# Performance work log

Hardware: AMD Instinct MI355X
Metric: run time of the kernel (lower is better)

The kernel has to match this reference:

```python
import jax, jax.numpy as jnp
import numpy as np

BN_EPS = 1e-5

def _bn(x, g, b, m, v):
    # eval-mode BatchNorm1d over channel dim of [B, C, N]
    scale = g / jnp.sqrt(v + BN_EPS)
    return (x - m[:, None]) * scale[:, None] + b[:, None]

def _conv1(W, x, b=None):
    # 1x1 Conv1d == channel matmul: W [O, C], x [B, C, N] -> [B, O, N]
    y = jnp.einsum('oc,bcn->bon', W, x)
    if b is not None:
        y = y + b[:, None]
    return y

def _sa_layer(x, wqk, wv, bv, wt, bt, g, b, m, v):
    # offset self-attention; q_conv and k_conv share weights
    xk = _conv1(wqk, x)                          # [B, D, N]
    xq = jnp.swapaxes(xk, 1, 2)                  # [B, N, D]
    xv = _conv1(wv, x, bv)                       # [B, D, N]
    energy = jnp.einsum('bnd,bdm->bnm', xq, xk)  # [B, N, N]
    attn = jax.nn.softmax(energy, axis=-1)
    attn = attn / (1e-9 + attn.sum(axis=1, keepdims=True))  # L1 renorm over dim=1
    x_r = jnp.einsum('bdn,bnm->bdm', xv, attn)   # [B, D, N]
    x_r = jax.nn.relu(_bn(_conv1(wt, x - x_r, bt), g, b, m, v))
    return x + x_r

def setup_inputs() -> dict:
    key = jax.random.key(0)
    ks = iter(jax.random.split(key, 64))
    B, Cin, N = 16, 3, 2048
    D, F, H1, OUT = 128, 1024, 512, 50
    def rn(shape, s=0.05):
        return jax.random.normal(next(ks), shape, dtype=jnp.float32) * s
    def var(shape):
        return jax.random.uniform(next(ks), shape, dtype=jnp.float32) * 0.5 + 0.5
    inp = {
        'x': jax.random.normal(next(ks), (B, Cin, N), dtype=jnp.float32),
        'w1': rn((D, Cin)), 'w2': rn((D, D)),
        'bn1_g': jnp.ones((D,)), 'bn1_b': jnp.zeros((D,)), 'bn1_m': rn((D,)), 'bn1_v': var((D,)),
        'bn2_g': jnp.ones((D,)), 'bn2_b': jnp.zeros((D,)), 'bn2_m': rn((D,)), 'bn2_v': var((D,)),
        'sa_wqk': rn((4, D, D)), 'sa_wv': rn((4, D, D)), 'sa_bv': rn((4, D)),
        'sa_wt': rn((4, D, D)), 'sa_bt': rn((4, D)),
        'sa_g': jnp.ones((4, D)), 'sa_b': jnp.zeros((4, D)), 'sa_m': rn((4, D)), 'sa_v': var((4, D)),
        'wf': rn((F, 4 * D)),
        'bnf_g': jnp.ones((F,)), 'bnf_b': jnp.zeros((F,)), 'bnf_m': rn((F,)), 'bnf_v': var((F,)),
        'ws1': rn((H1, 3 * F)), 'bs1': rn((H1,)),
        'bns1_g': jnp.ones((H1,)), 'bns1_b': jnp.zeros((H1,)), 'bns1_m': rn((H1,)), 'bns1_v': var((H1,)),
        'ws2': rn((OUT, H1)), 'bs2': rn((OUT,)),
        'bns2_g': jnp.ones((OUT,)), 'bns2_b': jnp.zeros((OUT,)), 'bns2_m': rn((OUT,)), 'bns2_v': var((OUT,)),
    }
    return inp

def reference(x, w1, w2, bn1_g, bn1_b, bn1_m, bn1_v, bn2_g, bn2_b, bn2_m, bn2_v,
              sa_wqk, sa_wv, sa_bv, sa_wt, sa_bt, sa_g, sa_b, sa_m, sa_v,
              wf, bnf_g, bnf_b, bnf_m, bnf_v,
              ws1, bs1, bns1_g, bns1_b, bns1_m, bns1_v,
              ws2, bs2, bns2_g, bns2_b, bns2_m, bns2_v):
    B, _, N = x.shape
    h = jax.nn.relu(_bn(_conv1(w1, x), bn1_g, bn1_b, bn1_m, bn1_v))
    h = jax.nn.relu(_bn(_conv1(w2, h), bn2_g, bn2_b, bn2_m, bn2_v))
    feats = []
    for i in range(4):
        h = _sa_layer(h, sa_wqk[i], sa_wv[i], sa_bv[i], sa_wt[i], sa_bt[i],
                      sa_g[i], sa_b[i], sa_m[i], sa_v[i])
        feats.append(h)
    cat = jnp.concatenate(feats, axis=1)                 # [B, 512, N]
    fused = _bn(_conv1(wf, cat), bnf_g, bnf_b, bnf_m, bnf_v)
    fused = jnp.where(fused >= 0, fused, 0.2 * fused)    # LeakyReLU(0.2)
    x_max = fused.max(axis=2)                            # [B, 1024]
    x_avg = fused.mean(axis=2)                           # [B, 1024]
    gmax = jnp.broadcast_to(x_max[:, :, None], (B, x_max.shape[1], N))
    gavg = jnp.broadcast_to(x_avg[:, :, None], (B, x_avg.shape[1], N))
    h = jnp.concatenate([fused, gmax, gavg], axis=1)     # [B, 3072, N]
    h = jax.nn.relu(_bn(_conv1(ws1, h, bs1), bns1_g, bns1_b, bns1_m, bns1_v))
    # dropout is identity in eval mode
    h = jax.nn.relu(_bn(_conv1(ws2, h, bs2), bns2_g, bns2_b, bns2_m, bns2_v))
    return h  # [B, out_channel, N]
```

## Files before the change

### kernel.cpp

```cpp
#include <hip/hip_runtime.h>
#include <cstdint>
#include <cstddef>

#define B_   16
#define N_   2048
#define D_   128
#define F_   1024
#define H1_  512
#define OUT_ 50

static constexpr float BN_EPS = 1e-5f;

typedef __attribute__((ext_vector_type(8))) short short8;
typedef __attribute__((ext_vector_type(4))) float f32x4;

__device__ inline unsigned short f2bf(float f) {
  union { float f; unsigned u; } v; v.f = f;
  unsigned r = v.u + 0x7fff + ((v.u >> 16) & 1);
  return (unsigned short)(r >> 16);
}
__device__ inline float bf2f(unsigned short h) {
  union { unsigned u; float f; } v; v.u = ((unsigned)h) << 16; return v.f;
}

__device__ inline void dma16(const unsigned short* g, unsigned short* l) {
  __builtin_amdgcn_global_load_lds(
      (const __attribute__((address_space(1))) unsigned int*)g,
      (__attribute__((address_space(3))) unsigned int*)l, 16, 0, 0);
}

__global__ void foldw_k(const float* __restrict__ W, int ldW,
                        const float* __restrict__ bias,
                        const float* __restrict__ g, const float* __restrict__ bb,
                        const float* __restrict__ m, const float* __restrict__ v,
                        unsigned short* __restrict__ Wb, float* __restrict__ biasF,
                        int O, int Opad, int K) {
  long i = (long)blockIdx.x * 256 + threadIdx.x;
  if (i >= (long)Opad * K) return;
  int o = (int)(i / K), k = (int)(i % K);
  float sc = 1.f, sh = 0.f;
  if (o < O && g) { sc = g[o] * rsqrtf(v[o] + BN_EPS); sh = bb[o] - m[o] * sc; }
  float w = (o < O) ? W[(long)o * ldW + k] * sc : 0.f;
  Wb[i] = f2bf(w);
  if (k == 0 && biasF) {
    float bf = 0.f;
    if (o < O) bf = (bias ? bias[o] : 0.f) * sc + sh;
    biasF[o] = bf;
  }
}

__global__ void conv1_k(const float* __restrict__ x, const float* __restrict__ w1,
                        const float* __restrict__ g, const float* __restrict__ bb,
                        const float* __restrict__ m, const float* __restrict__ v,
                        unsigned short* __restrict__ h0b) {
  int o = threadIdx.x, n = blockIdx.x, b = blockIdx.y;
  const float* xb = x + (long)b * 3 * N_;
  float val = w1[o * 3 + 0] * xb[n] + w1[o * 3 + 1] * xb[N_ + n] + w1[o * 3 + 2] * xb[2 * N_ + n];
  float sc = g[o] * rsqrtf(v[o] + BN_EPS);
  val = val * sc + (bb[o] - m[o] * sc);
  h0b[((long)b * N_ + n) * D_ + o] = f2bf(fmaxf(val, 0.f));
}

template <int TM>
__global__ __launch_bounds__(256, 4)
void gemm_tok(const unsigned short* __restrict__ Wb, int ldW,
              const unsigned short* __restrict__ A, long sA, int ldA,
              const float* __restrict__ biasF,
              const float* __restrict__ perBO, int ldPBO,
              const unsigned short* __restrict__ resH, long sRes, int ldRes,
              unsigned short* __restrict__ outH, long sOutH, int ldOutH,
              float* __restrict__ pmax, float* __restrict__ psum,
              int K, int act, int flags) {
  constexpr int MT = TM / 32;
  __shared__ unsigned short lAB[TM * 64 + 128 * 64];
  __shared__ float lpm[4][64], lps[4][64];
  unsigned short* lA = lAB;
  unsigned short* lB = lAB + TM * 64;
  unsigned short* lS = lAB;
  int tid = threadIdx.x;
  int n0 = blockIdx.x * TM, o0 = blockIdx.y * 128, b = blockIdx.z;
  int wave = tid >> 6, lane = tid & 63;
  int wr = wave >> 1, wc = wave & 1;
  int quad = lane >> 4, l15 = lane & 15;
  int rowL = lane >> 3;
  int kseg = (lane & 7) ^ rowL;
  const unsigned short* Ab = A + (long)b * sA + (long)n0 * ldA;
  const unsigned short* Wp = Wb + (long)o0 * ldW;

  f32x4 acc[MT][4];
  #pragma unroll
  for (int i = 0; i < MT; ++i)
    #pragma unroll
    for (int j = 0; j < 4; ++j) acc[i][j] = (f32x4){0.f, 0.f, 0.f, 0.f};

  for (int kc = 0; kc < K; kc += 64) {
    #pragma unroll
    for (int t = 0; t < 4; ++t) {
      int chunk = t * 4 + wave;
      dma16(Wp + (long)(chunk * 8 + rowL) * ldW + kc + kseg * 8, &lB[chunk * 512]);
      if (chunk < TM / 8)
        dma16(Ab + (long)(chunk * 8 + rowL) * ldA + kc + kseg * 8, &lA[chunk * 512]);
    }
    __syncthreads();
    #pragma unroll
    for (int kk = 0; kk < 2; ++kk) {
      short8 af[MT], bf[4];
      #pragma unroll
      for (int mt = 0; mt < MT; ++mt) {
        int r = wr * (TM / 2) + mt * 16 + l15;
        af[mt] = *(const short8*)&lA[r * 64 + (((kk * 4 + quad) ^ (l15 & 7)) * 8)];
      }
      #pragma unroll
      for (int ot = 0; ot < 4; ++ot) {
        int r = wc * 64 + ot * 16 + l15;
        bf[ot] = *(const short8*)&lB[r * 64 + (((kk * 4 + quad) ^ (l15 & 7)) * 8)];
      }
      #pragma unroll
      for (int mt = 0; mt < MT; ++mt)
        #pragma unroll
        for (int ot = 0; ot < 4; ++ot)
          acc[mt][ot] = __builtin_amdgcn_mfma_f32_16x16x32_bf16(bf[ot], af[mt], acc[mt][ot], 0, 0, 0);
    }
    __syncthreads();
  }

  bool doPool = (flags & 32) != 0;
  #pragma unroll
  for (int ot = 0; ot < 4; ++ot) {
    int obL = wc * 64 + ot * 16 + quad * 4;
    int ob = o0 + obL;
    float bi[4] = {0.f, 0.f, 0.f, 0.f};
    if (biasF) { float4 t = *(const float4*)&biasF[ob]; bi[0] = t.x; bi[1] = t.y; bi[2] = t.z; bi[3] = t.w; }
    if (perBO) {
      float4 t = *(const float4*)&perBO[(long)b * ldPBO + ob];
      bi[0] += t.x; bi[1] += t.y; bi[2] += t.z; bi[3] += t.w;
    }
    float pm4[4], ps4[4];
    #pragma unroll
    for (int r = 0; r < 4; ++r) { pm4[r] = -1e30f; ps4[r] = 0.f; }
    int g = obL >> 3, go = obL & 7;
    #pragma unroll
    for (int mt = 0; mt < MT; ++mt) {
      int nL = wr * (TM / 2) + mt * 16 + l15;
      float vals[4];
      #pragma unroll
      for (int r = 0; r < 4; ++r) {
        float val = acc[mt][ot][r] + bi[r];
        if (act == 1)      val = fmaxf(val, 0.f);
        else if (act == 2) val = (val >= 0.f) ? val : 0.2f * val;
        vals[r] = val;
      }
      if (flags & 16) {
        uint2 rv = *(const uint2*)&resH[(long)b * sRes + (long)(n0 + nL) * ldRes + ob];
        unsigned short rr[4];
        *(uint2*)rr = rv;
        #pragma unroll
        for (int r = 0; r < 4; ++r) vals[r] += bf2f(rr[r]);
      }
      unsigned short t4[4];
      #pragma unroll
      for (int r = 0; r < 4; ++r) {
        t4[r] = f2bf(vals[r]);
        if (doPool) { pm4[r] = fmaxf(pm4[r], vals[r]); ps4[r] += vals[r]; }
      }
      int gp = (g & 8) | ((g ^ (nL & 7)) & 7);
      *(uint2*)&lS[nL * 128 + gp * 8 + go] = *(uint2*)&t4[0];
    }
    if (doPool) {
      #pragma unroll
      for (int r = 0; r < 4; ++r) {
        float m = pm4[r], s = ps4[r];
        m = fmaxf(m, __shfl_xor(m, 1)); s += __shfl_xor(s, 1);
        m = fmaxf(m, __shfl_xor(m, 2)); s += __shfl_xor(s, 2);
        m = fmaxf(m, __shfl_xor(m, 4)); s += __shfl_xor(s, 4);
        m = fmaxf(m, __shfl_xor(m, 8)); s += __shfl_xor(s, 8);
        if (l15 == 0) { lpm[wave][ot * 16 + quad * 4 + r] = m; lps[wave][ot * 16 + quad * 4 + r] = s; }
      }
    }
  }
  __syncthreads();
  {
    int r0 = tid >> 4, s = tid & 15;
    #pragma unroll
    for (int it = 0; it < TM / 16; ++it) {
      int row = it * 16 + r0;
      int sp = (s & 8) | ((s ^ (row & 7)) & 7);
      short8 v = *(const short8*)&lS[row * 128 + sp * 8];
      *(short8*)&outH[(long)b * sOutH + (long)(n0 + row) * ldOutH + o0 + s * 8] = v;
    }
  }
  if (doPool && tid < 128) {
    int wcx = tid >> 6, ol = tid & 63;
    float m = fmaxf(lpm[wcx][ol], lpm[wcx + 2][ol]);
    float s = lps[wcx][ol] + lps[wcx + 2][ol];
    int o = o0 + wcx * 64 + ol;
    pmax[((long)b * 16 + blockIdx.x) * 1024 + o] = m;
    psum[((long)b * 16 + blockIdx.x) * 1024 + o] = s;
  }
}

template <int TM>
__global__ __launch_bounds__(256, 4)
void gemm_chan(const unsigned short* __restrict__ Wb, int ldW,
               const unsigned short* __restrict__ A, long sA, int ldA,
               const float* __restrict__ biasF,
               float* __restrict__ outF, long sOutF, int ldOutF,
               unsigned short* __restrict__ outH, long sOutH, int ldOutH,
               int K, int O, int act) {
  constexpr int MT = TM / 32;
  __shared__ unsigned short lA[TM * 64];
  __shared__ unsigned short lB[128 * 64];
  int tid = threadIdx.x;
  int n0 = blockIdx.x * TM, o0 = blockIdx.y * 128, b = blockIdx.z;
  int wave = tid >> 6, lane = tid & 63;
  int wr = wave >> 1, wc = wave & 1;
  int quad = lane >> 4, l15 = lane & 15;
  int rowL = lane >> 3;
  int kseg = (lane & 7) ^ rowL;
  const unsigned short* Ab = A + (long)b * sA + (long)n0 * ldA;
  const unsigned short* Wp = Wb + (long)o0 * ldW;

  f32x4 acc[MT][4];
  #pragma unroll
  for (int i = 0; i < MT; ++i)
    #pragma unroll
    for (int j = 0; j < 4; ++j) acc[i][j] = (f32x4){0.f, 0.f, 0.f, 0.f};

  for (int kc = 0; kc < K; kc += 64) {
    #pragma unroll
    for (int t = 0; t < 4; ++t) {
      int chunk = t * 4 + wave;
      dma16(Wp + (long)(chunk * 8 + rowL) * ldW + kc + kseg * 8, &lB[chunk * 512]);
      if (chunk < TM / 8)
        dma16(Ab + (long)(chunk * 8 + rowL) * ldA + kc + kseg * 8, &lA[chunk * 512]);
    }
    __syncthreads();
    #pragma unroll
    for (int kk = 0; kk < 2; ++kk) {
      short8 af[MT], bf[4];
      #pragma unroll
      for (int mt = 0; mt < MT; ++mt) {
        int r = wr * (TM / 2) + mt * 16 + l15;
        af[mt] = *(const short8*)&lA[r * 64 + (((kk * 4 + quad) ^ (l15 & 7)) * 8)];
      }
      #pragma unroll
      for (int ot = 0; ot < 4; ++ot) {
        int r = wc * 64 + ot * 16 + l15;
        bf[ot] = *(const short8*)&lB[r * 64 + (((kk * 4 + quad) ^ (l15 & 7)) * 8)];
      }
      #pragma unroll
      for (int mt = 0; mt < MT; ++mt)
        #pragma unroll
        for (int ot = 0; ot < 4; ++ot)
          acc[mt][ot] = __builtin_amdgcn_mfma_f32_16x16x32_bf16(af[mt], bf[ot], acc[mt][ot], 0, 0, 0);
    }
    __syncthreads();
  }

  #pragma unroll
  for (int ot = 0; ot < 4; ++ot) {
    int o = o0 + wc * 64 + ot * 16 + l15;
    if (o >= O) continue;
    float bi = biasF ? biasF[o] : 0.f;
    #pragma unroll
    for (int mt = 0; mt < MT; ++mt) {
      int nb = n0 + wr * (TM / 2) + mt * 16 + quad * 4;
      float vals[4];
      #pragma unroll
      for (int r = 0; r < 4; ++r) {
        float val = acc[mt][ot][r] + bi;
        if (act == 1)      val = fmaxf(val, 0.f);
        else if (act == 2) val = (val >= 0.f) ? val : 0.2f * val;
        vals[r] = val;
      }
      if (outF)
        *(float4*)&outF[(long)b * sOutF + (long)o * ldOutF + nb] = *(float4*)vals;
      if (outH) {
        unsigned short t[4];
        #pragma unroll
        for (int r = 0; r < 4; ++r) t[r] = f2bf(vals[r]);
        *(uint2*)&outH[(long)b * sOutH + (long)o * ldOutH + nb] = *(uint2*)&t[0];
      }
    }
  }
}

__global__ __launch_bounds__(256)
void gram_lw(const unsigned short* __restrict__ xk, long sXk,
             float* __restrict__ lw) {
  __shared__ unsigned short lK[2][64 * 128];
  int tid = threadIdx.x, wave = tid >> 6, lane = tid & 63;
  int quad = lane >> 4, l15 = lane & 15;
  int rowL4 = lane >> 4, s16 = lane & 15;
  int n0 = blockIdx.y * 64, b = blockIdx.x;
  const unsigned short* Kp = xk + (long)b * sXk;
  short8 afr[4];
  {
    const unsigned short* arow = Kp + (long)(n0 + wave * 16 + l15) * 128;
    #pragma unroll
    for (int kf = 0; kf < 4; ++kf) afr[kf] = *(const short8*)(arow + kf * 32 + quad * 8);
  }
  float runm[4], runs[4];
  #pragma unroll
  for (int r = 0; r < 4; ++r) { runm[r] = -1e30f; runs[r] = 0.f; }

  auto stage = [&](int ch, int bf) {
    #pragma unroll
    for (int t = 0; t < 4; ++t) {
      int c = t * 4 + wave;
      int row = c * 4 + rowL4;
      int gseg = (s16 & 8) | ((s16 ^ (row & 7)) & 7);
      dma16(Kp + (long)(ch * 64 + row) * 128 + gseg * 8, &lK[bf][c * 512]);
    }
  };
  stage(0, 0);

  for (int ch = 0; ch < 32; ++ch) {
    __syncthreads();
    int bf = ch & 1;
    if (ch + 1 < 32) stage(ch + 1, bf ^ 1);
    f32x4 sv[4];
    #pragma unroll
    for (int mf = 0; mf < 4; ++mf) {
      f32x4 s = (f32x4){0.f, 0.f, 0.f, 0.f};
      #pragma unroll
      for (int kf = 0; kf < 4; ++kf) {
        int r = mf * 16 + l15, q = kf * 4 + quad;
        int sp = (q & 8) | ((q ^ (r & 7)) & 7);
        short8 bfr = *(const short8*)&lK[bf][r * 128 + sp * 8];
        s = __builtin_amdgcn_mfma_f32_16x16x32_bf16(afr[kf], bfr, s, 0, 0, 0);
      }
      sv[mf] = s;
    }
    #pragma unroll
    for (int r = 0; r < 4; ++r) {
      float e0 = sv[0][r], e1 = sv[1][r], e2 = sv[2][r], e3 = sv[3][r];
      float cm = fmaxf(fmaxf(e0, e1), fmaxf(e2, e3));
      float mn = fmaxf(runm[r], cm);
      runs[r] = runs[r] * __expf(runm[r] - mn) +
                (__expf(e0 - mn) + __expf(e1 - mn)) + (__expf(e2 - mn) + __expf(e3 - mn));
      runm[r] = mn;
    }
  }
  #pragma unroll
  for (int r = 0; r < 4; ++r) {
    float m = runm[r], s = runs[r];
    #pragma unroll
    for (int off = 1; off < 16; off <<= 1) {
      float mo = __shfl_xor(m, off), so = __shfl_xor(s, off);
      float mn = fmaxf(m, mo);
      s = s * __expf(m - mn) + so * __expf(mo - mn);
      m = mn;
    }
    if (l15 == 0) {
      int n = n0 + wave * 16 + quad * 4 + r;
      lw[(long)b * 2048 + n] = m + __logf(s);
    }
  }
}

__global__ __launch_bounds__(256)
void pv_k(const unsigned short* __restrict__ xk, long sXk,
          const unsigned short* __restrict__ xv, long sXv,
          const float* __restrict__ lw,
          const unsigned short* __restrict__ lib, long sLi, int ldLi,
          unsigned short* __restrict__ xrb, long sXr) {
  __shared__ unsigned short lK[2][64 * 128];
  __shared__ unsigned short lV[2][128 * 64];
  __shared__ unsigned short lP[4][16 * 64];
  __shared__ float lwt[2][64];
  int tid = threadIdx.x, wave = tid >> 6, lane = tid & 63;
  int quad = lane >> 4, l15 = lane & 15;
  int rowL4 = lane >> 4, s16 = lane & 15;
  int rowL8 = lane >> 3, s8 = lane & 7;
  int m0 = blockIdx.y * 64, b = blockIdx.x;
  const unsigned short* Kp = xk + (long)b * sXk;
  const unsigned short* Vp = xv + (long)b * sXv;
  short8 akr[4];
  {
    const unsigned short* arow = Kp + (long)(m0 + wave * 16 + l15) * 128;
    #pragma unroll
    for (int kf = 0; kf < 4; ++kf) akr[kf] = *(const short8*)(arow + kf * 32 + quad * 8);
  }
  f32x4 acc[8];
  #pragma unroll
  for (int dt = 0; dt < 8; ++dt) acc[dt] = (f32x4){0.f, 0.f, 0.f, 0.f};
  float runc[4] = {0.f, 0.f, 0.f, 0.f};

  auto stage = [&](int ch, int bf) {
    #pragma unroll
    for (int t = 0; t < 4; ++t) {
      int c = t * 4 + wave;
      int rowK = c * 4 + rowL4;
      int gsegK = (s16 & 8) | ((s16 ^ (rowK & 7)) & 7);
      dma16(Kp + (long)(ch * 64 + rowK) * 128 + gsegK * 8, &lK[bf][c * 512]);
      int rowV = c * 8 + rowL8;
      int gsegV = s8 ^ (rowV & 7);
      dma16(Vp + (long)rowV * 2048 + ch * 64 + gsegV * 8, &lV[bf][c * 512]);
    }
    if (tid < 64) lwt[bf][tid] = lw[(long)b * 2048 + ch * 64 + tid];
  };
  stage(0, 0);

  for (int ch = 0; ch < 32; ++ch) {
    __syncthreads();
    int bf = ch & 1;
    if (ch + 1 < 32) stage(ch + 1, bf ^ 1);
    #pragma unroll
    for (int nf = 0; nf < 4; ++nf) {
      f32x4 s = (f32x4){0.f, 0.f, 0.f, 0.f};
      #pragma unroll
      for (int kf = 0; kf < 4; ++kf) {
        int r = nf * 16 + l15, q = kf * 4 + quad;
        int sp = (q & 8) | ((q ^ (r & 7)) & 7);
        short8 bfr = *(const short8*)&lK[bf][r * 128 + sp * 8];
        s = __builtin_amdgcn_mfma_f32_16x16x32_bf16(akr[kf], bfr, s, 0, 0, 0);
      }
      float lwc = lwt[bf][nf * 16 + l15];
      int segIn = nf * 2 + (l15 >> 3);
      #pragma unroll
      for (int r = 0; r < 4; ++r) {
        float p = __expf(s[r] - lwc);
        runc[r] += p;
        int row = quad * 4 + r;
        int seg = (segIn ^ (row & 7)) & 7;
        lP[wave][row * 64 + seg * 8 + (l15 & 7)] = f2bf(p);
      }
    }
    #pragma unroll
    for (int kc = 0; kc < 2; ++kc) {
      int qp = kc * 4 + quad;
      short8 pa = *(const short8*)&lP[wave][l15 * 64 + ((qp ^ (l15 & 7)) & 7) * 8];
      #pragma unroll
      for (int dt = 0; dt < 8; ++dt) {
        int r = dt * 16 + l15;
        int sp = qp ^ (r & 7);
        short8 vb = *(const short8*)&lV[bf][r * 64 + sp * 8];
        acc[dt] = __builtin_amdgcn_mfma_f32_16x16x32_bf16(pa, vb, acc[dt], 0, 0, 0);
      }
    }
  }
  float inv[4];
  #pragma unroll
  for (int r = 0; r < 4; ++r) {
    float s = runc[r];
    #pragma unroll
    for (int off = 1; off < 16; off <<= 1) s += __shfl_xor(s, off);
    inv[r] = 1.f / (1e-9f + s);
  }
  #pragma unroll
  for (int dt = 0; dt < 8; ++dt) {
    int d = dt * 16 + l15;
    #pragma unroll
    for (int r = 0; r < 4; ++r) {
      int m = m0 + wave * 16 + quad * 4 + r;
      float lv = bf2f(lib[(long)b * sLi + (long)m * ldLi + d]);
      xrb[(long)b * sXr + (long)m * 128 + d] = f2bf(lv - acc[dt][r] * inv[r]);
    }
  }
}

__global__ void poolred_k(const float* __restrict__ pmax, const float* __restrict__ psum,
                          float* __restrict__ xmax, float* __restrict__ xavg) {
  int f = blockIdx.x * 256 + threadIdx.x, b = blockIdx.y;
  float mx = -1e30f, s = 0.f;
  #pragma unroll
  for (int t = 0; t < 16; ++t) {
    mx = fmaxf(mx, pmax[((long)b * 16 + t) * 1024 + f]);
    s += psum[((long)b * 16 + t) * 1024 + f];
  }
  xmax[(long)b * 1024 + f] = mx;
  xavg[(long)b * 1024 + f] = s * (1.f / 2048.f);
}

__global__ __launch_bounds__(256)
void poolterm_k(const float* __restrict__ ws1, const float* __restrict__ xmax,
                const float* __restrict__ xavg,
                const float* __restrict__ bg, const float* __restrict__ bv,
                float* __restrict__ pt) {
  int o = blockIdx.x, b = blockIdx.y, tid = threadIdx.x;
  const float* w = ws1 + (long)o * 3072;
  float s = 0.f;
  #pragma unroll
  for (int it = 0; it < 4; ++it) {
    int c = tid + it * 256;
    s += w[1024 + c] * xmax[(long)b * 1024 + c] + w[2048 + c] * xavg[(long)b * 1024 + c];
  }
  #pragma unroll
  for (int off = 32; off; off >>= 1) s += __shfl_xor(s, off);
  __shared__ float rsm[4];
  if ((tid & 63) == 0) rsm[tid >> 6] = s;
  __syncthreads();
  if (tid == 0) {
    float sc = bg[o] * rsqrtf(bv[o] + BN_EPS);
    pt[(long)b * H1_ + o] = sc * (rsm[0] + rsm[1] + rsm[2] + rsm[3]);
  }
}

extern "C" void kernel_launch(void* const* d_in, const int* in_sizes, int n_in,
                              void* d_out, int out_size, void* d_ws, size_t ws_size,
                              hipStream_t stream) {
  const float* x      = (const float*)d_in[0];
  const float* w1     = (const float*)d_in[1];
  const float* w2     = (const float*)d_in[2];
  const float* bn1_g  = (const float*)d_in[3];
  const float* bn1_b  = (const float*)d_in[4];
  const float* bn1_m  = (const float*)d_in[5];
  const float* bn1_v  = (const float*)d_in[6];
  const float* bn2_g  = (const float*)d_in[7];
  const float* bn2_b  = (const float*)d_in[8];
  const float* bn2_m  = (const float*)d_in[9];
  const float* bn2_v  = (const float*)d_in[10];
  const float* sa_wqk = (const float*)d_in[11];
  const float* sa_wv  = (const float*)d_in[12];
  const float* sa_bv  = (const float*)d_in[13];
  const float* sa_wt  = (const float*)d_in[14];
  const float* sa_bt  = (const float*)d_in[15];
  const float* sa_g   = (const float*)d_in[16];
  const float* sa_b   = (const float*)d_in[17];
  const float* sa_m   = (const float*)d_in[18];
  const float* sa_v   = (const float*)d_in[19];
  const float* wf     = (const float*)d_in[20];
  const float* bnf_g  = (const float*)d_in[21];
  const float* bnf_b  = (const float*)d_in[22];
  const float* bnf_m  = (const float*)d_in[23];
  const float* bnf_v  = (const float*)d_in[24];
  const float* ws1    = (const float*)d_in[25];
  const float* bs1    = (const float*)d_in[26];
  const float* bns1_g = (const float*)d_in[27];
  const float* bns1_b = (const float*)d_in[28];
  const float* bns1_m = (const float*)d_in[29];
  const float* bns1_v = (const float*)d_in[30];
  const float* ws2    = (const float*)d_in[31];
  const float* bs2    = (const float*)d_in[32];
  const float* bns2_g = (const float*)d_in[33];
  const float* bns2_b = (const float*)d_in[34];
  const float* bns2_m = (const float*)d_in[35];
  const float* bns2_v = (const float*)d_in[36];
  float* out = (float*)d_out;

  float* ws = (float*)d_ws;
  size_t off = 0;
  auto alloc  = [&](size_t n) { float* p = ws + off; off += (n + 63) & ~(size_t)63; return p; };
  auto allocH = [&](size_t n) { return (unsigned short*)alloc((n + 1) / 2); };

  unsigned short* w2b  = allocH(128 * 128);
  unsigned short* wqkb = allocH(4 * 128 * 128);
  unsigned short* wvb  = allocH(4 * 128 * 128);
  unsigned short* wtb  = allocH(4 * 128 * 128);
  unsigned short* wfb  = allocH((size_t)F_ * 512);
  unsigned short* ws1b = allocH((size_t)H1_ * 1024);
  unsigned short* ws2b = allocH((size_t)128 * 512);
  float* bias_w2 = alloc(128);
  float* bias_v  = alloc(512);
  float* bias_t  = alloc(512);
  float* bias_f  = alloc(1024);
  float* bias_s1 = alloc(512);
  float* bias_s2 = alloc(128);
  float* lwB  = alloc((size_t)16 * 2048);
  float* pmax = alloc((size_t)16 * 16 * 1024);
  float* psum = alloc((size_t)16 * 16 * 1024);
  float* xmaxB = alloc((size_t)16 * 1024);
  float* xavgB = alloc((size_t)16 * 1024);
  float* ptB   = alloc((size_t)16 * 512);
  size_t fixedOff = off;

  const size_t perB = 131072 + 524288 + 1048576 + 131072 + 131072 + 131072;
  size_t wsFloats = ws_size / 4;
  int Gb = 1;
  for (int c : {16, 8, 4, 2, 1}) {
    if (fixedOff + (size_t)c * perB + 4096 <= wsFloats) { Gb = c; break; }
  }

  unsigned short* h1b    = allocH((size_t)Gb * 262144);
  unsigned short* featsb = allocH((size_t)Gb * 1048576);
  unsigned short* fusedb = allocH((size_t)Gb * 2097152);
  unsigned short* xkb    = allocH((size_t)Gb * 262144);
  unsigned short* xvb    = allocH((size_t)Gb * 262144);
  unsigned short* xrb    = allocH((size_t)Gb * 262144);
  unsigned short* h0b  = xrb;
  unsigned short* hs1b = featsb;

  foldw_k<<<64, 256, 0, stream>>>(w2, 128, nullptr, bn2_g, bn2_b, bn2_m, bn2_v,
                                  w2b, bias_w2, 128, 128, 128);
  for (int i = 0; i < 4; ++i) {
    foldw_k<<<64, 256, 0, stream>>>(sa_wqk + (size_t)i * 16384, 128, nullptr,
                                    nullptr, nullptr, nullptr, nullptr,
                                    wqkb + (size_t)i * 16384, nullptr, 128, 128, 128);
    foldw_k<<<64, 256, 0, stream>>>(sa_wv + (size_t)i * 16384, 128, sa_bv + i * 128,
                                    nullptr, nullptr, nullptr, nullptr,
                                    wvb + (size_t)i * 16384, bias_v + i * 128, 128, 128, 128);
    foldw_k<<<64, 256, 0, stream>>>(sa_wt + (size_t)i * 16384, 128, sa_bt + i * 128,
                                    sa_g + i * 128, sa_b + i * 128, sa_m + i * 128, sa_v + i * 128,
                                    wtb + (size_t)i * 16384, bias_t + i * 128, 128, 128, 128);
  }
  foldw_k<<<2048, 256, 0, stream>>>(wf, 512, nullptr, bnf_g, bnf_b, bnf_m, bnf_v,
                                    wfb, bias_f, 1024, 1024, 512);
  foldw_k<<<2048, 256, 0, stream>>>(ws1, 3072, bs1, bns1_g, bns1_b, bns1_m, bns1_v,
                                    ws1b, bias_s1, 512, 512, 1024);
  foldw_k<<<256, 256, 0, stream>>>(ws2, 512, bs2, bns2_g, bns2_b, bns2_m, bns2_v,
                                   ws2b, bias_s2, 50, 128, 512);

  const long sAct = 262144, sFeat = 1048576, sFus = 2097152;
  for (int b0 = 0; b0 < B_; b0 += Gb) {
    int g = Gb;
    conv1_k<<<dim3(N_, g), 128, 0, stream>>>(x + (long)b0 * 3 * N_, w1,
                                             bn1_g, bn1_b, bn1_m, bn1_v, h0b);
    gemm_tok<64><<<dim3(32, 1, g), 256, 0, stream>>>(
        w2b, 128, h0b, sAct, 128, bias_w2, nullptr, 0, nullptr, 0, 0,
        h1b, sAct, 128, nullptr, nullptr, 128, 1, 0);

    for (int i = 0; i < 4; ++i) {
      const unsigned short* lib = (i == 0) ? h1b : featsb + (size_t)(i - 1) * 128;
      int ldLi = (i == 0) ? 128 : 512;
      long sLi = (i == 0) ? sAct : sFeat;
      gemm_tok<64><<<dim3(32, 1, g), 256, 0, stream>>>(
          wqkb + (size_t)i * 16384, 128, lib, sLi, ldLi, nullptr, nullptr, 0,
          nullptr, 0, 0, xkb, sAct, 128, nullptr, nullptr, 128, 0, 0);
      gemm_chan<64><<<dim3(32, 1, g), 256, 0, stream>>>(
          wvb + (size_t)i * 16384, 128, lib, sLi, ldLi, bias_v + i * 128,
          nullptr, 0, 0, xvb, sAct, 2048, 128, 128, 0);
      gram_lw<<<dim3(g, 32), 256, 0, stream>>>(xkb, sAct, lwB);
      pv_k<<<dim3(g, 32), 256, 0, stream>>>(xkb, sAct, xvb, sAct, lwB,
                                            lib, sLi, ldLi, xrb, sAct);
      gemm_tok<64><<<dim3(32, 1, g), 256, 0, stream>>>(
          wtb + (size_t)i * 16384, 128, xrb, sAct, 128, bias_t + i * 128, nullptr, 0,
          lib, sLi, ldLi,
          featsb + (size_t)i * 128, sFeat, 512, nullptr, nullptr, 128, 1, 16);
    }

    gemm_tok<128><<<dim3(16, 8, g), 256, 0, stream>>>(
        wfb, 512, featsb, sFeat, 512, bias_f, nullptr, 0, nullptr, 0, 0,
        fusedb, sFus, 1024, pmax, psum, 512, 2, 32);
    poolred_k<<<dim3(4, g), 256, 0, stream>>>(pmax, psum, xmaxB, xavgB);
    poolterm_k<<<dim3(512, g), 256, 0, stream>>>(ws1, xmaxB, xavgB, bns1_g, bns1_v, ptB);
    gemm_tok<128><<<dim3(16, 4, g), 256, 0, stream>>>(
        ws1b, 1024, fusedb, sFus, 1024, bias_s1, ptB, 512, nullptr, 0, 0,
        hs1b, sFeat, 512, nullptr, nullptr, 1024, 1, 0);
    gemm_chan<64><<<dim3(32, 1, g), 256, 0, stream>>>(
        ws2b, 512, hs1b, sFeat, 512, bias_s2,
        out + (long)b0 * OUT_ * N_, (long)OUT_ * N_, 2048, nullptr, 0, 0,
        512, 50, 1);
  }
}
```

Baseline: 782.6 us.

## Materialize bf16 energy matrix in gram pass and reuse it in PV kernel

The gram/logsumexp kernel now also writes the full N×N energy matrix in bf16 (transposed) to workspace. The PV kernel then streams those energies instead of recomputing QK^T with MFMA, which also removes the per-wave LDS round trip for P. This trades recomputation for a large extra global write and read per batch, 8 MB per batch per layer, and it enlarges the workspace so fewer batches may fit per group. Energies are also rounded to bf16 before the exponential, which lowers precision.

```diff
diff --git a/kernel.cpp b/kernel.cpp
--- a/kernel.cpp
+++ b/kernel.cpp
@@ -287,13 +287,14 @@
 
 __global__ __launch_bounds__(256)
 void gram_lw(const unsigned short* __restrict__ xk, long sXk,
-             float* __restrict__ lw) {
+             float* __restrict__ lw, unsigned short* __restrict__ eT) {
   __shared__ unsigned short lK[2][64 * 128];
   int tid = threadIdx.x, wave = tid >> 6, lane = tid & 63;
   int quad = lane >> 4, l15 = lane & 15;
   int rowL4 = lane >> 4, s16 = lane & 15;
   int n0 = blockIdx.y * 64, b = blockIdx.x;
   const unsigned short* Kp = xk + (long)b * sXk;
+  unsigned short* eTp = eT + (long)b * 4194304;
   short8 afr[4];
   {
     const unsigned short* arow = Kp + (long)(n0 + wave * 16 + l15) * 128;
@@ -331,6 +332,14 @@
         s = __builtin_amdgcn_mfma_f32_16x16x32_bf16(afr[kf], bfr, s, 0, 0, 0);
       }
       sv[mf] = s;
+    }
+    #pragma unroll
+    for (int mf = 0; mf < 4; ++mf) {
+      unsigned short t4[4];
+      #pragma unroll
+      for (int r = 0; r < 4; ++r) t4[r] = f2bf(sv[mf][r]);
+      long mrow = (long)(ch * 64 + mf * 16 + l15);
+      *(uint2*)&eTp[mrow * 2048 + n0 + wave * 16 + quad * 4] = *(uint2*)&t4[0];
     }
     #pragma unroll
     for (int r = 0; r < 4; ++r) {
@@ -360,40 +369,36 @@
 }
 
 __global__ __launch_bounds__(256)
-void pv_k(const unsigned short* __restrict__ xk, long sXk,
+void pv_k(const unsigned short* __restrict__ eT,
           const unsigned short* __restrict__ xv, long sXv,
           const float* __restrict__ lw,
           const unsigned short* __restrict__ lib, long sLi, int ldLi,
           unsigned short* __restrict__ xrb, long sXr) {
-  __shared__ unsigned short lK[2][64 * 128];
+  __shared__ unsigned short lE[2][64 * 64];
   __shared__ unsigned short lV[2][128 * 64];
-  __shared__ unsigned short lP[4][16 * 64];
   __shared__ float lwt[2][64];
   int tid = threadIdx.x, wave = tid >> 6, lane = tid & 63;
   int quad = lane >> 4, l15 = lane & 15;
-  int rowL4 = lane >> 4, s16 = lane & 15;
   int rowL8 = lane >> 3, s8 = lane & 7;
   int m0 = blockIdx.y * 64, b = blockIdx.x;
-  const unsigned short* Kp = xk + (long)b * sXk;
+  const unsigned short* Ep = eT + (long)b * 4194304 + (long)m0 * 2048;
   const unsigned short* Vp = xv + (long)b * sXv;
-  short8 akr[4];
-  {
-    const unsigned short* arow = Kp + (long)(m0 + wave * 16 + l15) * 128;
-    #pragma unroll
-    for (int kf = 0; kf < 4; ++kf) akr[kf] = *(const short8*)(arow + kf * 32 + quad * 8);
-  }
   f32x4 acc[8];
   #pragma unroll
   for (int dt = 0; dt < 8; ++dt) acc[dt] = (f32x4){0.f, 0.f, 0.f, 0.f};
-  float runc[4] = {0.f, 0.f, 0.f, 0.f};
+  float runc = 0.f;
 
   auto stage = [&](int ch, int bf) {
+    #pragma unroll
+    for (int t = 0; t < 2; ++t) {
+      int c = t * 4 + wave;
+      int rowE = c * 8 + rowL8;
+      int gseg = s8 ^ (rowE & 7);
+      dma16(Ep + (long)rowE * 2048 + ch * 64 + gseg * 8, &lE[bf][c * 512]);
+    }
     #pragma unroll
     for (int t = 0; t < 4; ++t) {
       int c = t * 4 + wave;
-      int rowK = c * 4 + rowL4;
-      int gsegK = (s16 & 8) | ((s16 ^ (rowK & 7)) & 7);
-      dma16(Kp + (long)(ch * 64 + rowK) * 128 + gsegK * 8, &lK[bf][c * 512]);
       int rowV = c * 8 + rowL8;
       int gsegV = s8 ^ (rowV & 7);
       dma16(Vp + (long)rowV * 2048 + ch * 64 + gsegV * 8, &lV[bf][c * 512]);
@@ -402,52 +407,43 @@
   };
   stage(0, 0);
 
+  int rowm = wave * 16 + l15;
   for (int ch = 0; ch < 32; ++ch) {
     __syncthreads();
     int bf = ch & 1;
     if (ch + 1 < 32) stage(ch + 1, bf ^ 1);
     #pragma unroll
-    for (int nf = 0; nf < 4; ++nf) {
-      f32x4 s = (f32x4){0.f, 0.f, 0.f, 0.f};
-      #pragma unroll
-      for (int kf = 0; kf < 4; ++kf) {
-        int r = nf * 16 + l15, q = kf * 4 + quad;
-        int sp = (q & 8) | ((q ^ (r & 7)) & 7);
-        short8 bfr = *(const short8*)&lK[bf][r * 128 + sp * 8];
-        s = __builtin_amdgcn_mfma_f32_16x16x32_bf16(akr[kf], bfr, s, 0, 0, 0);
-      }
-      float lwc = lwt[bf][nf * 16 + l15];
-      int segIn = nf * 2 + (l15 >> 3);
-      #pragma unroll
-      for (int r = 0; r < 4; ++r) {
-        float p = __expf(s[r] - lwc);
-        runc[r] += p;
-        int row = quad * 4 + r;
-        int seg = (segIn ^ (row & 7)) & 7;
-        lP[wave][row * 64 + seg * 8 + (l15 & 7)] = f2bf(p);
-      }
-    }
-    #pragma unroll
     for (int kc = 0; kc < 2; ++kc) {
-      int qp = kc * 4 + quad;
-      short8 pa = *(const short8*)&lP[wave][l15 * 64 + ((qp ^ (l15 & 7)) & 7) * 8];
+      int sp = (kc * 4 + quad) ^ (l15 & 7);
+      short8 e8 = *(const short8*)&lE[bf][rowm * 64 + sp * 8];
+      const float* lp = &lwt[bf][kc * 32 + quad * 8];
+      float4 w0 = *(const float4*)lp;
+      float4 w1 = *(const float4*)(lp + 4);
+      float lwv[8] = {w0.x, w0.y, w0.z, w0.w, w1.x, w1.y, w1.z, w1.w};
+      unsigned short pb[8];
+      #pragma unroll
+      for (int j = 0; j < 8; ++j) {
+        float p = __expf(bf2f((unsigned short)e8[j]) - lwv[j]);
+        runc += p;
+        pb[j] = f2bf(p);
+      }
+      short8 pa = *(short8*)&pb[0];
       #pragma unroll
       for (int dt = 0; dt < 8; ++dt) {
         int r = dt * 16 + l15;
-        int sp = qp ^ (r & 7);
-        short8 vb = *(const short8*)&lV[bf][r * 64 + sp * 8];
+        int spv = (kc * 4 + quad) ^ (r & 7);
+        short8 vb = *(const short8*)&lV[bf][r * 64 + spv * 8];
         acc[dt] = __builtin_amdgcn_mfma_f32_16x16x32_bf16(pa, vb, acc[dt], 0, 0, 0);
       }
     }
   }
-  float inv[4];
-  #pragma unroll
-  for (int r = 0; r < 4; ++r) {
-    float s = runc[r];
-    #pragma unroll
-    for (int off = 1; off < 16; off <<= 1) s += __shfl_xor(s, off);
-    inv[r] = 1.f / (1e-9f + s);
-  }
+  float s = runc;
+  s += __shfl_xor(s, 16);
+  s += __shfl_xor(s, 32);
+  float inv = 1.f / (1e-9f + s);
+  float inv4[4];
+  #pragma unroll
+  for (int r = 0; r < 4; ++r) inv4[r] = __shfl(inv, quad * 4 + r);
   #pragma unroll
   for (int dt = 0; dt < 8; ++dt) {
     int d = dt * 16 + l15;
@@ -455,7 +451,7 @@
     for (int r = 0; r < 4; ++r) {
       int m = m0 + wave * 16 + quad * 4 + r;
       float lv = bf2f(lib[(long)b * sLi + (long)m * ldLi + d]);
-      xrb[(long)b * sXr + (long)m * 128 + d] = f2bf(lv - acc[dt][r] * inv[r]);
+      xrb[(long)b * sXr + (long)m * 128 + d] = f2bf(lv - acc[dt][r] * inv4[r]);
     }
   }
 }
@@ -565,7 +561,7 @@
   float* ptB   = alloc((size_t)16 * 512);
   size_t fixedOff = off;
 
-  const size_t perB = 131072 + 524288 + 1048576 + 131072 + 131072 + 131072;
+  const size_t perB = 131072 + 524288 + 1048576 + 131072 + 131072 + 131072 + 2097152;
   size_t wsFloats = ws_size / 4;
   int Gb = 1;
   for (int c : {16, 8, 4, 2, 1}) {
@@ -578,6 +574,7 @@
   unsigned short* xkb    = allocH((size_t)Gb * 262144);
   unsigned short* xvb    = allocH((size_t)Gb * 262144);
   unsigned short* xrb    = allocH((size_t)Gb * 262144);
+  unsigned short* eTb    = allocH((size_t)Gb * 4194304);
   unsigned short* h0b  = xrb;
   unsigned short* hs1b = featsb;
 
@@ -620,8 +617,8 @@
       gemm_chan<64><<<dim3(32, 1, g), 256, 0, stream>>>(
           wvb + (size_t)i * 16384, 128, lib, sLi, ldLi, bias_v + i * 128,
           nullptr, 0, 0, xvb, sAct, 2048, 128, 128, 0);
-      gram_lw<<<dim3(g, 32), 256, 0, stream>>>(xkb, sAct, lwB);
-      pv_k<<<dim3(g, 32), 256, 0, stream>>>(xkb, sAct, xvb, sAct, lwB,
+      gram_lw<<<dim3(g, 32), 256, 0, stream>>>(xkb, sAct, lwB, eTb);
+      pv_k<<<dim3(g, 32), 256, 0, stream>>>(eTb, xvb, sAct, lwB,
                                             lib, sLi, ldLi, xrb, sAct);
       gemm_tok<64><<<dim3(32, 1, g), 256, 0, stream>>>(
           wtb + (size_t)i * 16384, 128, xrb, sAct, 128, bias_t + i * 128, nullptr, 0,
```

Result: slower. 1.106 ms (+41.3%).
